# Performance work log

Hardware: AMD Instinct MI355X
Metric: run time of the kernel (lower is better)

The kernel has to match this reference:

```python
import jax, jax.numpy as jnp
import numpy as np

B = 256          # graphs per batch
N = 128          # nodes per graph (equal-size graphs; batch is block-contiguous)
P = N * (N - 1) // 2  # pairs per graph = 8128
E = B * 1024     # total edges
D = 128          # node feature dim
L = 32           # latent dim

# precomputed local upper-triangular pair indices (constants)
_PI, _PJ = np.triu_indices(N, k=1)
_PI = jnp.asarray(_PI); _PJ = jnp.asarray(_PJ)


def setup_inputs() -> dict:
    key = jax.random.key(0)
    ks = jax.random.split(key, 8)
    x = jax.random.normal(ks[0], (B * N, D), dtype=jnp.float32)
    # within-graph edges with local i < j
    li = jax.random.randint(ks[1], (E,), 0, N - 1)
    r = jax.random.randint(ks[2], (E,), 0, 1 << 30)
    lj = li + 1 + r % (N - 1 - li)
    g = jax.random.randint(ks[3], (E,), 0, B)
    off = g * N
    edge_index = jnp.stack([off + li, off + lj]).astype(jnp.int64)
    batch = jnp.repeat(jnp.arange(B), N).astype(jnp.int64)
    eps = jax.random.normal(ks[4], (B * N, L), dtype=jnp.float32)
    W1 = jax.random.normal(ks[5], (D, D), dtype=jnp.float32) * 0.05
    b1 = jnp.zeros((D,), dtype=jnp.float32)
    Wmu = jax.random.normal(ks[6], (D, L), dtype=jnp.float32) * 0.05
    bmu = jnp.zeros((L,), dtype=jnp.float32)
    Wls = jax.random.normal(ks[7], (D, L), dtype=jnp.float32) * 0.05
    bls = jnp.zeros((L,), dtype=jnp.float32)
    return {"x": x, "edge_index": edge_index, "batch": batch, "eps": eps,
            "W1": W1, "b1": b1, "Wmu": Wmu, "bmu": bmu, "Wls": Wls, "bls": bls}


def reference(x, edge_index, batch, eps, W1, b1, Wmu, bmu, Wls, bls):
    src, dst = edge_index[0], edge_index[1]
    # --- encoder: one symmetric message-passing layer -> Gaussian q per node ---
    agg = jnp.zeros_like(x).at[dst].add(x[src]).at[src].add(x[dst])
    h = jax.nn.relu((x + agg) @ W1 + b1)
    mu = h @ Wmu + bmu                       # [BN, L]
    log_std = h @ Wls + bls
    std = jnp.exp(log_std)
    z = mu + std * eps                       # rsample
    # --- KL(q || N(0,I)) per node, summed per graph (kls[b]) ---
    kl_node = 0.5 * jnp.sum(std * std + mu * mu - 1.0 - 2.0 * log_std, axis=-1)
    kls = jax.ops.segment_sum(kl_node, batch, num_segments=B)  # [B]
    # --- link targets: scatter edges into triangular pair slots ---
    li, lj, be = src % N, dst % N, src // N
    pidx = li * (2 * N - li - 1) // 2 + (lj - li - 1)
    targets = jnp.zeros((B, P), dtype=z.dtype).at[be, pidx].set(1.0)
    # --- inner-product Bernoulli decoder over all pairs of every graph ---
    zb = z.reshape(B, N, L)
    logits = jnp.einsum('bpl,bpl->bp', zb[:, _PI], zb[:, _PJ])   # [B, P]
    log_probs = jnp.sum(targets * logits - jax.nn.softplus(logits), axis=-1)  # [B]
    elbo = jnp.mean(log_probs - kls)
    return -elbo
```

## Files before the change

### kernel.cpp

```cpp
#include <hip/hip_runtime.h>
#include <math.h>

#define B_ 256
#define N_ 128
#define D_ 128
#define L_ 32
#define E_ 262144
#define PW_ 254
#define DCAP 96

#define NDEG_OFF 0
#define BM_OFF   32768
#define KLS_OFF  97792
#define LP_OFF   98048
#define ADJ_OFF  98304
#define Z_OFF    884736
#define ZERO_WORDS 98304

__global__ __launch_bounds__(256) void k_build(
    const int* __restrict__ ei, unsigned* __restrict__ ndeg,
    unsigned char* __restrict__ adj, unsigned* __restrict__ bm)
{
    int e = blockIdx.x * 256 + threadIdx.x;
    int src = ei[e], dst = ei[E_ + e];
    unsigned s1 = atomicAdd(&ndeg[src], 1u);
    if (s1 < DCAP) adj[(size_t)src * DCAP + s1] = (unsigned char)(dst & 127);
    unsigned s2 = atomicAdd(&ndeg[dst], 1u);
    if (s2 < DCAP) adj[(size_t)dst * DCAP + s2] = (unsigned char)(src & 127);
    int li = src & 127, lj = dst & 127, g = src >> 7;
    int p = li * (255 - li) / 2 + (lj - li - 1);
    atomicOr(&bm[g * PW_ + (p >> 5)], 1u << (p & 31));
}

__global__ __launch_bounds__(256, 4) void k_encoder(
    const float* __restrict__ x, const unsigned* __restrict__ ndeg,
    const unsigned char* __restrict__ adj,
    const float* __restrict__ W1, const float* __restrict__ b1,
    const float* __restrict__ Wmu, const float* __restrict__ bmu,
    const float* __restrict__ Wls, const float* __restrict__ bls,
    const float* __restrict__ eps,
    float* __restrict__ z, float* __restrict__ kls)
{
    __shared__ float XAs[32 * 132];
    __shared__ float Ws[4096];
    int t = threadIdx.x;
    int g = blockIdx.x & 255;
    int quar = blockIdx.x >> 8;
    int row0 = g * 128 + quar * 32;
    int rg = t >> 5;
    int cg = t & 31;
    int lane = t & 63;

    {
        int nidx = t >> 4;
        int fo = (t & 15) * 8;
        for (int p = 0; p < 2; ++p) {
            int lrow = p * 16 + nidx;
            int gnode = row0 + lrow;
            const float* xr = x + (size_t)gnode * 128 + fo;
            float4 a0 = *(const float4*)xr;
            float4 a1 = *(const float4*)(xr + 4);
            int deg = (int)ndeg[gnode];
            if (deg > DCAP) deg = DCAP;
            const unsigned char* al = adj + (size_t)gnode * DCAP;
            const float* gx = x + (size_t)(gnode & ~127) * 128 + fo;
            int e = 0;
            for (; e + 4 <= deg; e += 4) {
                unsigned pk = *(const unsigned*)(al + e);
                const float* r0 = gx + (pk & 255u) * 128;
                const float* r1 = gx + ((pk >> 8) & 255u) * 128;
                const float* r2 = gx + ((pk >> 16) & 255u) * 128;
                const float* r3 = gx + (pk >> 24) * 128;
                float4 v00 = *(const float4*)r0, v01 = *(const float4*)(r0 + 4);
                float4 v10 = *(const float4*)r1, v11 = *(const float4*)(r1 + 4);
                float4 v20 = *(const float4*)r2, v21 = *(const float4*)(r2 + 4);
                float4 v30 = *(const float4*)r3, v31 = *(const float4*)(r3 + 4);
                a0.x += v00.x + v10.x + v20.x + v30.x;
                a0.y += v00.y + v10.y + v20.y + v30.y;
                a0.z += v00.z + v10.z + v20.z + v30.z;
                a0.w += v00.w + v10.w + v20.w + v30.w;
                a1.x += v01.x + v11.x + v21.x + v31.x;
                a1.y += v01.y + v11.y + v21.y + v31.y;
                a1.z += v01.z + v11.z + v21.z + v31.z;
                a1.w += v01.w + v11.w + v21.w + v31.w;
            }
            for (; e < deg; ++e) {
                const float* r = gx + (unsigned)al[e] * 128;
                float4 v0 = *(const float4*)r, v1 = *(const float4*)(r + 4);
                a0.x += v0.x; a0.y += v0.y; a0.z += v0.z; a0.w += v0.w;
                a1.x += v1.x; a1.y += v1.y; a1.z += v1.z; a1.w += v1.w;
            }
            *(float4*)(XAs + lrow * 132 + fo) = a0;
            *(float4*)(XAs + lrow * 132 + fo + 4) = a1;
        }
    }
    __syncthreads();

    float acc[4][4];
    #pragma unroll
    for (int i = 0; i < 4; ++i)
        #pragma unroll
        for (int j = 0; j < 4; ++j) acc[i][j] = 0.f;

    for (int kq = 0; kq < 4; ++kq) {
        if (kq) __syncthreads();
        #pragma unroll
        for (int i = 0; i < 4; ++i) {
            int c = t + i * 256;
            ((float4*)Ws)[c] = ((const float4*)(W1 + kq * 4096))[c];
        }
        __syncthreads();
        #pragma unroll 2
        for (int k = 0; k < 32; k += 4) {
            float4 av[4], wv[4];
            #pragma unroll
            for (int i = 0; i < 4; ++i)
                av[i] = *(const float4*)(XAs + (4 * rg + i) * 132 + kq * 32 + k);
            #pragma unroll
            for (int dk = 0; dk < 4; ++dk)
                wv[dk] = *(const float4*)(Ws + (k + dk) * 128 + 4 * cg);
            #pragma unroll
            for (int i = 0; i < 4; ++i) {
                acc[i][0] += av[i].x * wv[0].x + av[i].y * wv[1].x + av[i].z * wv[2].x + av[i].w * wv[3].x;
                acc[i][1] += av[i].x * wv[0].y + av[i].y * wv[1].y + av[i].z * wv[2].y + av[i].w * wv[3].y;
                acc[i][2] += av[i].x * wv[0].z + av[i].y * wv[1].z + av[i].z * wv[2].z + av[i].w * wv[3].z;
                acc[i][3] += av[i].x * wv[0].w + av[i].y * wv[1].w + av[i].z * wv[2].w + av[i].w * wv[3].w;
            }
        }
    }
    __syncthreads();

    {
        float4 bb = *(const float4*)(b1 + 4 * cg);
        #pragma unroll
        for (int i = 0; i < 4; ++i) {
            float4 h;
            h.x = fmaxf(acc[i][0] + bb.x, 0.f);
            h.y = fmaxf(acc[i][1] + bb.y, 0.f);
            h.z = fmaxf(acc[i][2] + bb.z, 0.f);
            h.w = fmaxf(acc[i][3] + bb.w, 0.f);
            *(float4*)(XAs + (4 * rg + i) * 132 + 4 * cg) = h;
        }
    }

    float a3[4][2];
    #pragma unroll
    for (int i = 0; i < 4; ++i) { a3[i][0] = 0.f; a3[i][1] = 0.f; }

    for (int kh = 0; kh < 2; ++kh) {
        __syncthreads();
        #pragma unroll
        for (int i = 0; i < 4; ++i) {
            int c = t + i * 256;
            int row = c >> 4, col4 = (c & 15) << 2;
            int rowg = kh * 64 + row;
            float4 v = (col4 < 32) ? *(const float4*)(Wmu + rowg * 32 + col4)
                                   : *(const float4*)(Wls + rowg * 32 + col4 - 32);
            *(float4*)(Ws + row * 64 + col4) = v;
        }
        __syncthreads();
        #pragma unroll 2
        for (int k = 0; k < 64; k += 4) {
            float4 av[4];
            float2 wv[4];
            #pragma unroll
            for (int i = 0; i < 4; ++i)
                av[i] = *(const float4*)(XAs + (4 * rg + i) * 132 + kh * 64 + k);
            #pragma unroll
            for (int dk = 0; dk < 4; ++dk)
                wv[dk] = *(const float2*)(Ws + (k + dk) * 64 + 2 * cg);
            #pragma unroll
            for (int i = 0; i < 4; ++i) {
                a3[i][0] += av[i].x * wv[0].x + av[i].y * wv[1].x + av[i].z * wv[2].x + av[i].w * wv[3].x;
                a3[i][1] += av[i].x * wv[0].y + av[i].y * wv[1].y + av[i].z * wv[2].y + av[i].w * wv[3].y;
            }
        }
    }
    {
        float2 bv = (cg < 16) ? *(const float2*)(bmu + 2 * cg)
                              : *(const float2*)(bls + 2 * cg - 32);
        #pragma unroll
        for (int i = 0; i < 4; ++i) { a3[i][0] += bv.x; a3[i][1] += bv.y; }
    }

    float o3[4][2];
    #pragma unroll
    for (int i = 0; i < 4; ++i) {
        o3[i][0] = __shfl_xor(a3[i][0], 16);
        o3[i][1] = __shfl_xor(a3[i][1], 16);
    }

    float klsum = 0.f;
    if (cg < 16) {
        int lo = cg;
        #pragma unroll
        for (int i = 0; i < 4; ++i) {
            int rowg = row0 + 4 * rg + i;
            float mu0 = a3[i][0], mu1 = a3[i][1];
            float ls0 = o3[i][0], ls1 = o3[i][1];
            float2 ev = *(const float2*)(eps + (size_t)rowg * 32 + 2 * lo);
            float s0 = __expf(ls0), s1 = __expf(ls1);
            float2 zv = make_float2(mu0 + s0 * ev.x, mu1 + s1 * ev.y);
            *(float2*)(z + (size_t)rowg * 32 + 2 * lo) = zv;
            klsum += s0 * s0 + mu0 * mu0 - 1.f - 2.f * ls0
                   + s1 * s1 + mu1 * mu1 - 1.f - 2.f * ls1;
        }
    }
    #pragma unroll
    for (int off = 32; off > 0; off >>= 1) klsum += __shfl_xor(klsum, off);
    if (lane == 0) atomicAdd(&kls[g], 0.5f * klsum);
}

__global__ __launch_bounds__(256) void k_decoder(
    const float* __restrict__ z, const unsigned* __restrict__ bitmap,
    float* __restrict__ logp)
{
    __shared__ float zT[32 * 132];
    __shared__ unsigned bm[PW_];
    int b = blockIdx.x & 255, quar = blockIdx.x >> 8, t = threadIdx.x;

    #pragma unroll
    for (int i = 0; i < 16; ++i) {
        int c = t + i * 256;
        int n = c >> 5, l = c & 31;
        zT[l * 132 + n] = z[((size_t)b * N_ + n) * L_ + l];
    }
    if (t < PW_) bm[t] = bitmap[b * PW_ + t];
    __syncthreads();

    int i0 = quar * 32 + ((t >> 5) << 2);
    int j0 = (t & 31) << 2;
    float g[4][4];
    #pragma unroll
    for (int a = 0; a < 4; ++a)
        #pragma unroll
        for (int c = 0; c < 4; ++c) g[a][c] = 0.f;

    #pragma unroll 4
    for (int l = 0; l < 32; ++l) {
        float4 a0 = *(const float4*)(zT + l * 132 + i0);
        float4 b0 = *(const float4*)(zT + l * 132 + j0);
        float za[4] = {a0.x, a0.y, a0.z, a0.w};
        float zb[4] = {b0.x, b0.y, b0.z, b0.w};
        #pragma unroll
        for (int a = 0; a < 4; ++a)
            #pragma unroll
            for (int c = 0; c < 4; ++c) g[a][c] += za[a] * zb[c];
    }

    float sum = 0.f;
    #pragma unroll
    for (int a = 0; a < 4; ++a) {
        int i = i0 + a;
        #pragma unroll
        for (int c = 0; c < 4; ++c) {
            int j = j0 + c;
            if (j > i) {
                float lg = g[a][c];
                int p = i * (255 - i) / 2 + (j - i - 1);
                unsigned bit = (bm[p >> 5] >> (p & 31)) & 1u;
                float sp = __logf(1.f + __expf(-fabsf(lg))) + fmaxf(lg, 0.f);
                sum += bit ? (lg - sp) : (-sp);
            }
        }
    }
    #pragma unroll
    for (int off = 32; off > 0; off >>= 1) sum += __shfl_xor(sum, off);
    if ((t & 63) == 0) atomicAdd(&logp[b], sum);
}

__global__ __launch_bounds__(256) void k_finalize(
    const float* __restrict__ kls, const float* __restrict__ logp,
    float* __restrict__ out)
{
    __shared__ float RED[256];
    int t = threadIdx.x;
    RED[t] = logp[t] - kls[t];
    __syncthreads();
    for (int s = 128; s > 0; s >>= 1) {
        if (t < s) RED[t] += RED[t + s];
        __syncthreads();
    }
    if (t == 0) out[0] = -RED[0] * (1.0f / 256.0f);
}

extern "C" void kernel_launch(void* const* d_in, const int* in_sizes, int n_in,
                              void* d_out, int out_size, void* d_ws, size_t ws_size,
                              hipStream_t stream) {
    const float* x   = (const float*)d_in[0];
    const int*   ei  = (const int*)d_in[1];
    const float* eps = (const float*)d_in[3];
    const float* W1  = (const float*)d_in[4];
    const float* b1  = (const float*)d_in[5];
    const float* Wmu = (const float*)d_in[6];
    const float* bmu = (const float*)d_in[7];
    const float* Wls = (const float*)d_in[8];
    const float* bls = (const float*)d_in[9];

    unsigned* wsw = (unsigned*)d_ws;
    unsigned*      ndeg = wsw + NDEG_OFF;
    unsigned*      bm   = wsw + BM_OFF;
    float*         kls  = (float*)(wsw + KLS_OFF);
    float*         logp = (float*)(wsw + LP_OFF);
    unsigned char* adj  = (unsigned char*)(wsw + ADJ_OFF);
    float*         z    = (float*)(wsw + Z_OFF);

    hipMemsetAsync(d_ws, 0, ZERO_WORDS * sizeof(unsigned), stream);

    k_build   <<<E_ / 256, 256, 0, stream>>>(ei, ndeg, adj, bm);
    k_encoder <<<1024, 256, 0, stream>>>(x, ndeg, adj, W1, b1, Wmu, bmu,
                                         Wls, bls, eps, z, kls);
    k_decoder <<<4 * B_, 256, 0, stream>>>(z, bm, logp);
    k_finalize<<<1, 256, 0, stream>>>(kls, logp, (float*)d_out);
}
```

Baseline: 177.5 us.

## Replace neighbor gather with dense adjacency matmul and fuse finalize into decoder

The encoder no longer gathers neighbor feature rows per edge. It builds a 32x128 local (A+I) count matrix in shared memory with LDS atomics and computes (A+I)·X as a dense matmul over the graph's 128 node rows, then multiplies by W1. This turns the irregular gather loads into coalesced tile loads, at the cost of an extra 32x128x128 matmul per block. The separate finalize kernel is removed: the last decoder block, found through a global atomic counter, does the final reduction, which saves one launch.

```diff
diff --git a/kernel.cpp b/kernel.cpp
--- a/kernel.cpp
+++ b/kernel.cpp
@@ -13,9 +13,10 @@
 #define BM_OFF   32768
 #define KLS_OFF  97792
 #define LP_OFF   98048
-#define ADJ_OFF  98304
-#define Z_OFF    884736
-#define ZERO_WORDS 98304
+#define CNT_OFF  98304
+#define ADJ_OFF  98320
+#define Z_OFF    884752
+#define ZERO_WORDS 98320
 
 __global__ __launch_bounds__(256) void k_build(
     const int* __restrict__ ei, unsigned* __restrict__ ndeg,
@@ -41,7 +42,7 @@
     const float* __restrict__ eps,
     float* __restrict__ z, float* __restrict__ kls)
 {
-    __shared__ float XAs[32 * 132];
+    __shared__ float As[32 * 132];
     __shared__ float Ws[4096];
     int t = threadIdx.x;
     int g = blockIdx.x & 255;
@@ -52,47 +53,19 @@
     int lane = t & 63;
 
     {
-        int nidx = t >> 4;
-        int fo = (t & 15) * 8;
-        for (int p = 0; p < 2; ++p) {
-            int lrow = p * 16 + nidx;
-            int gnode = row0 + lrow;
-            const float* xr = x + (size_t)gnode * 128 + fo;
-            float4 a0 = *(const float4*)xr;
-            float4 a1 = *(const float4*)(xr + 4);
-            int deg = (int)ndeg[gnode];
-            if (deg > DCAP) deg = DCAP;
-            const unsigned char* al = adj + (size_t)gnode * DCAP;
-            const float* gx = x + (size_t)(gnode & ~127) * 128 + fo;
-            int e = 0;
-            for (; e + 4 <= deg; e += 4) {
-                unsigned pk = *(const unsigned*)(al + e);
-                const float* r0 = gx + (pk & 255u) * 128;
-                const float* r1 = gx + ((pk >> 8) & 255u) * 128;
-                const float* r2 = gx + ((pk >> 16) & 255u) * 128;
-                const float* r3 = gx + (pk >> 24) * 128;
-                float4 v00 = *(const float4*)r0, v01 = *(const float4*)(r0 + 4);
-                float4 v10 = *(const float4*)r1, v11 = *(const float4*)(r1 + 4);
-                float4 v20 = *(const float4*)r2, v21 = *(const float4*)(r2 + 4);
-                float4 v30 = *(const float4*)r3, v31 = *(const float4*)(r3 + 4);
-                a0.x += v00.x + v10.x + v20.x + v30.x;
-                a0.y += v00.y + v10.y + v20.y + v30.y;
-                a0.z += v00.z + v10.z + v20.z + v30.z;
-                a0.w += v00.w + v10.w + v20.w + v30.w;
-                a1.x += v01.x + v11.x + v21.x + v31.x;
-                a1.y += v01.y + v11.y + v21.y + v31.y;
-                a1.z += v01.z + v11.z + v21.z + v31.z;
-                a1.w += v01.w + v11.w + v21.w + v31.w;
-            }
-            for (; e < deg; ++e) {
-                const float* r = gx + (unsigned)al[e] * 128;
-                float4 v0 = *(const float4*)r, v1 = *(const float4*)(r + 4);
-                a0.x += v0.x; a0.y += v0.y; a0.z += v0.z; a0.w += v0.w;
-                a1.x += v1.x; a1.y += v1.y; a1.z += v1.z; a1.w += v1.w;
-            }
-            *(float4*)(XAs + lrow * 132 + fo) = a0;
-            *(float4*)(XAs + lrow * 132 + fo + 4) = a1;
-        }
+        float4 z4 = make_float4(0.f, 0.f, 0.f, 0.f);
+        for (int c = t; c < 1056; c += 256) ((float4*)As)[c] = z4;
+    }
+    __syncthreads();
+    {
+        int nd = t >> 3, sub = t & 7;
+        int gnode = row0 + nd;
+        int deg = (int)ndeg[gnode];
+        if (deg > DCAP) deg = DCAP;
+        const unsigned char* al = adj + (size_t)gnode * DCAP;
+        if (sub == 0) As[nd * 132 + quar * 32 + nd] = 1.0f;
+        for (int e = sub; e < deg; e += 8)
+            atomicAdd(&As[nd * 132 + (int)al[e]], 1.0f);
     }
     __syncthreads();
 
@@ -102,12 +75,13 @@
         #pragma unroll
         for (int j = 0; j < 4; ++j) acc[i][j] = 0.f;
 
-    for (int kq = 0; kq < 4; ++kq) {
-        if (kq) __syncthreads();
+    for (int kc = 0; kc < 4; ++kc) {
+        if (kc) __syncthreads();
+        const float* xg = x + ((size_t)(g * 128 + kc * 32)) * 128;
         #pragma unroll
         for (int i = 0; i < 4; ++i) {
             int c = t + i * 256;
-            ((float4*)Ws)[c] = ((const float4*)(W1 + kq * 4096))[c];
+            ((float4*)Ws)[c] = ((const float4*)xg)[c];
         }
         __syncthreads();
         #pragma unroll 2
@@ -115,7 +89,7 @@
             float4 av[4], wv[4];
             #pragma unroll
             for (int i = 0; i < 4; ++i)
-                av[i] = *(const float4*)(XAs + (4 * rg + i) * 132 + kq * 32 + k);
+                av[i] = *(const float4*)(As + (4 * rg + i) * 132 + kc * 32 + k);
             #pragma unroll
             for (int dk = 0; dk < 4; ++dk)
                 wv[dk] = *(const float4*)(Ws + (k + dk) * 128 + 4 * cg);
@@ -129,6 +103,43 @@
         }
     }
     __syncthreads();
+    #pragma unroll
+    for (int i = 0; i < 4; ++i)
+        *(float4*)(As + (4 * rg + i) * 132 + 4 * cg) =
+            make_float4(acc[i][0], acc[i][1], acc[i][2], acc[i][3]);
+
+    #pragma unroll
+    for (int i = 0; i < 4; ++i)
+        #pragma unroll
+        for (int j = 0; j < 4; ++j) acc[i][j] = 0.f;
+
+    for (int kq = 0; kq < 4; ++kq) {
+        __syncthreads();
+        #pragma unroll
+        for (int i = 0; i < 4; ++i) {
+            int c = t + i * 256;
+            ((float4*)Ws)[c] = ((const float4*)(W1 + kq * 4096))[c];
+        }
+        __syncthreads();
+        #pragma unroll 2
+        for (int k = 0; k < 32; k += 4) {
+            float4 av[4], wv[4];
+            #pragma unroll
+            for (int i = 0; i < 4; ++i)
+                av[i] = *(const float4*)(As + (4 * rg + i) * 132 + kq * 32 + k);
+            #pragma unroll
+            for (int dk = 0; dk < 4; ++dk)
+                wv[dk] = *(const float4*)(Ws + (k + dk) * 128 + 4 * cg);
+            #pragma unroll
+            for (int i = 0; i < 4; ++i) {
+                acc[i][0] += av[i].x * wv[0].x + av[i].y * wv[1].x + av[i].z * wv[2].x + av[i].w * wv[3].x;
+                acc[i][1] += av[i].x * wv[0].y + av[i].y * wv[1].y + av[i].z * wv[2].y + av[i].w * wv[3].y;
+                acc[i][2] += av[i].x * wv[0].z + av[i].y * wv[1].z + av[i].z * wv[2].z + av[i].w * wv[3].z;
+                acc[i][3] += av[i].x * wv[0].w + av[i].y * wv[1].w + av[i].z * wv[2].w + av[i].w * wv[3].w;
+            }
+        }
+    }
+    __syncthreads();
 
     {
         float4 bb = *(const float4*)(b1 + 4 * cg);
@@ -139,7 +150,7 @@
             h.y = fmaxf(acc[i][1] + bb.y, 0.f);
             h.z = fmaxf(acc[i][2] + bb.z, 0.f);
             h.w = fmaxf(acc[i][3] + bb.w, 0.f);
-            *(float4*)(XAs + (4 * rg + i) * 132 + 4 * cg) = h;
+            *(float4*)(As + (4 * rg + i) * 132 + 4 * cg) = h;
         }
     }
 
@@ -165,7 +176,7 @@
             float2 wv[4];
             #pragma unroll
             for (int i = 0; i < 4; ++i)
-                av[i] = *(const float4*)(XAs + (4 * rg + i) * 132 + kh * 64 + k);
+                av[i] = *(const float4*)(As + (4 * rg + i) * 132 + kh * 64 + k);
             #pragma unroll
             for (int dk = 0; dk < 4; ++dk)
                 wv[dk] = *(const float2*)(Ws + (k + dk) * 64 + 2 * cg);
@@ -213,10 +224,12 @@
 
 __global__ __launch_bounds__(256) void k_decoder(
     const float* __restrict__ z, const unsigned* __restrict__ bitmap,
-    float* __restrict__ logp)
+    const float* __restrict__ kls, float* __restrict__ logp,
+    unsigned* __restrict__ cnt, float* __restrict__ out)
 {
     __shared__ float zT[32 * 132];
     __shared__ unsigned bm[PW_];
+    __shared__ unsigned sOld;
     int b = blockIdx.x & 255, quar = blockIdx.x >> 8, t = threadIdx.x;
 
     #pragma unroll
@@ -267,21 +280,23 @@
     #pragma unroll
     for (int off = 32; off > 0; off >>= 1) sum += __shfl_xor(sum, off);
     if ((t & 63) == 0) atomicAdd(&logp[b], sum);
-}
-
-__global__ __launch_bounds__(256) void k_finalize(
-    const float* __restrict__ kls, const float* __restrict__ logp,
-    float* __restrict__ out)
-{
-    __shared__ float RED[256];
-    int t = threadIdx.x;
-    RED[t] = logp[t] - kls[t];
-    __syncthreads();
-    for (int s = 128; s > 0; s >>= 1) {
-        if (t < s) RED[t] += RED[t + s];
-        __syncthreads();
-    }
-    if (t == 0) out[0] = -RED[0] * (1.0f / 256.0f);
+
+    __syncthreads();
+    if (t == 0) { __threadfence(); sOld = atomicAdd(cnt, 1u); }
+    __syncthreads();
+    if (sOld == 4 * B_ - 1) {
+        __threadfence();
+        float lp = atomicAdd(&logp[t], 0.0f);
+        float kv = kls[t];
+        float* RED = zT;
+        RED[t] = lp - kv;
+        __syncthreads();
+        for (int s = 128; s > 0; s >>= 1) {
+            if (t < s) RED[t] += RED[t + s];
+            __syncthreads();
+        }
+        if (t == 0) out[0] = -RED[0] * (1.0f / 256.0f);
+    }
 }
 
 extern "C" void kernel_launch(void* const* d_in, const int* in_sizes, int n_in,
@@ -302,6 +317,7 @@
     unsigned*      bm   = wsw + BM_OFF;
     float*         kls  = (float*)(wsw + KLS_OFF);
     float*         logp = (float*)(wsw + LP_OFF);
+    unsigned*      cnt  = wsw + CNT_OFF;
     unsigned char* adj  = (unsigned char*)(wsw + ADJ_OFF);
     float*         z    = (float*)(wsw + Z_OFF);
 
@@ -310,6 +326,5 @@
     k_build   <<<E_ / 256, 256, 0, stream>>>(ei, ndeg, adj, bm);
     k_encoder <<<1024, 256, 0, stream>>>(x, ndeg, adj, W1, b1, Wmu, bmu,
                                          Wls, bls, eps, z, kls);
-    k_decoder <<<4 * B_, 256, 0, stream>>>(z, bm, logp);
-    k_finalize<<<1, 256, 0, stream>>>(kls, logp, (float*)d_out);
+    k_decoder <<<4 * B_, 256, 0, stream>>>(z, bm, kls, logp, cnt, (float*)d_out);
 }
```

Result: slower. 192.6 us (+8.5%).

## Double-buffer encoder weight tiles with async global-to-LDS loads

Applied to the files above, without the earlier changes.

Replaces the synchronous register-staged copies of W1 and the fused Wmu/Wls tiles with `global_load_lds` direct-to-LDS transfers into a two-slot shared buffer. The next weight chunk is now issued before the current one is consumed, and the first W1 chunk is issued before neighbour aggregation. The goal is to hide weight-load latency behind the FMA loops and the gather, and to cut a barrier per chunk. In exchange, chunks are smaller (16 rows), so there are more iterations. Correctness depends on the compiler waiting on the outstanding async loads before each barrier.

```diff
diff --git a/kernel.cpp b/kernel.cpp
--- a/kernel.cpp
+++ b/kernel.cpp
@@ -16,6 +16,12 @@
 #define ADJ_OFF  98304
 #define Z_OFF    884736
 #define ZERO_WORDS 98304
+
+typedef const float __attribute__((address_space(1)))* gas_ptr;
+typedef float __attribute__((address_space(3)))* las_ptr;
+__device__ __forceinline__ void dma16(const float* g, float* l) {
+    __builtin_amdgcn_global_load_lds((gas_ptr)g, (las_ptr)l, 16, 0, 0);
+}
 
 __global__ __launch_bounds__(256) void k_build(
     const int* __restrict__ ei, unsigned* __restrict__ ndeg,
@@ -42,7 +48,7 @@
     float* __restrict__ z, float* __restrict__ kls)
 {
     __shared__ float XAs[32 * 132];
-    __shared__ float Ws[4096];
+    __shared__ float Ws[2][2048];
     int t = threadIdx.x;
     int g = blockIdx.x & 255;
     int quar = blockIdx.x >> 8;
@@ -50,6 +56,13 @@
     int rg = t >> 5;
     int cg = t & 31;
     int lane = t & 63;
+    int w = t >> 6;
+
+    int seg0 = w * 128 + (t & 63);
+    int seg1 = seg0 + 64;
+
+    dma16(W1 + 4 * seg0, Ws[0] + 4 * (w * 128));
+    dma16(W1 + 4 * seg1, Ws[0] + 4 * (w * 128 + 64));
 
     {
         int nidx = t >> 4;
@@ -102,23 +115,32 @@
         #pragma unroll
         for (int j = 0; j < 4; ++j) acc[i][j] = 0.f;
 
-    for (int kq = 0; kq < 4; ++kq) {
-        if (kq) __syncthreads();
-        #pragma unroll
-        for (int i = 0; i < 4; ++i) {
-            int c = t + i * 256;
-            ((float4*)Ws)[c] = ((const float4*)(W1 + kq * 4096))[c];
-        }
-        __syncthreads();
-        #pragma unroll 2
-        for (int k = 0; k < 32; k += 4) {
+    for (int c = 0; c < 8; ++c) {
+        if (c < 7) {
+            const float* src = W1 + (c + 1) * 2048;
+            float* dst = Ws[(c + 1) & 1];
+            dma16(src + 4 * seg0, dst + 4 * (w * 128));
+            dma16(src + 4 * seg1, dst + 4 * (w * 128 + 64));
+        } else {
+            float* dst = Ws[0];
+            int c0 = seg0, c1 = seg1;
+            int r0_ = c0 >> 4, k0 = (c0 & 15) << 2;
+            int r1_ = c1 >> 4, k1 = (c1 & 15) << 2;
+            const float* s0 = (k0 < 32) ? Wmu + r0_ * 32 + k0 : Wls + r0_ * 32 + k0 - 32;
+            const float* s1 = (k1 < 32) ? Wmu + r1_ * 32 + k1 : Wls + r1_ * 32 + k1 - 32;
+            dma16(s0, dst + 4 * (w * 128));
+            dma16(s1, dst + 4 * (w * 128 + 64));
+        }
+        const float* WsC = Ws[c & 1];
+        #pragma unroll
+        for (int k = 0; k < 16; k += 4) {
             float4 av[4], wv[4];
             #pragma unroll
             for (int i = 0; i < 4; ++i)
-                av[i] = *(const float4*)(XAs + (4 * rg + i) * 132 + kq * 32 + k);
+                av[i] = *(const float4*)(XAs + (4 * rg + i) * 132 + c * 16 + k);
             #pragma unroll
             for (int dk = 0; dk < 4; ++dk)
-                wv[dk] = *(const float4*)(Ws + (k + dk) * 128 + 4 * cg);
+                wv[dk] = *(const float4*)(WsC + (k + dk) * 128 + 4 * cg);
             #pragma unroll
             for (int i = 0; i < 4; ++i) {
                 acc[i][0] += av[i].x * wv[0].x + av[i].y * wv[1].x + av[i].z * wv[2].x + av[i].w * wv[3].x;
@@ -127,8 +149,8 @@
                 acc[i][3] += av[i].x * wv[0].w + av[i].y * wv[1].w + av[i].z * wv[2].w + av[i].w * wv[3].w;
             }
         }
-    }
-    __syncthreads();
+        __syncthreads();
+    }
 
     {
         float4 bb = *(const float4*)(b1 + 4 * cg);
@@ -142,39 +164,41 @@
             *(float4*)(XAs + (4 * rg + i) * 132 + 4 * cg) = h;
         }
     }
+    __syncthreads();
 
     float a3[4][2];
     #pragma unroll
     for (int i = 0; i < 4; ++i) { a3[i][0] = 0.f; a3[i][1] = 0.f; }
 
-    for (int kh = 0; kh < 2; ++kh) {
-        __syncthreads();
-        #pragma unroll
-        for (int i = 0; i < 4; ++i) {
-            int c = t + i * 256;
-            int row = c >> 4, col4 = (c & 15) << 2;
-            int rowg = kh * 64 + row;
-            float4 v = (col4 < 32) ? *(const float4*)(Wmu + rowg * 32 + col4)
-                                   : *(const float4*)(Wls + rowg * 32 + col4 - 32);
-            *(float4*)(Ws + row * 64 + col4) = v;
-        }
-        __syncthreads();
+    for (int q = 0; q < 4; ++q) {
+        if (q < 3) {
+            float* dst = Ws[(q + 1) & 1];
+            int c0 = seg0, c1 = seg1;
+            int r0_ = (q + 1) * 32 + (c0 >> 4), k0 = (c0 & 15) << 2;
+            int r1_ = (q + 1) * 32 + (c1 >> 4), k1 = (c1 & 15) << 2;
+            const float* s0 = (k0 < 32) ? Wmu + r0_ * 32 + k0 : Wls + r0_ * 32 + k0 - 32;
+            const float* s1 = (k1 < 32) ? Wmu + r1_ * 32 + k1 : Wls + r1_ * 32 + k1 - 32;
+            dma16(s0, dst + 4 * (w * 128));
+            dma16(s1, dst + 4 * (w * 128 + 64));
+        }
+        const float* WsC = Ws[q & 1];
         #pragma unroll 2
-        for (int k = 0; k < 64; k += 4) {
+        for (int k = 0; k < 32; k += 4) {
             float4 av[4];
             float2 wv[4];
             #pragma unroll
             for (int i = 0; i < 4; ++i)
-                av[i] = *(const float4*)(XAs + (4 * rg + i) * 132 + kh * 64 + k);
+                av[i] = *(const float4*)(XAs + (4 * rg + i) * 132 + q * 32 + k);
             #pragma unroll
             for (int dk = 0; dk < 4; ++dk)
-                wv[dk] = *(const float2*)(Ws + (k + dk) * 64 + 2 * cg);
+                wv[dk] = *(const float2*)(WsC + (k + dk) * 64 + 2 * cg);
             #pragma unroll
             for (int i = 0; i < 4; ++i) {
                 a3[i][0] += av[i].x * wv[0].x + av[i].y * wv[1].x + av[i].z * wv[2].x + av[i].w * wv[3].x;
                 a3[i][1] += av[i].x * wv[0].y + av[i].y * wv[1].y + av[i].z * wv[2].y + av[i].w * wv[3].y;
             }
         }
+        if (q < 3) __syncthreads();
     }
     {
         float2 bv = (cg < 16) ? *(const float2*)(bmu + 2 * cg)
```

New measurement: 210.3 us. +18.5%, slower.
